# Optimization experiments

Measured on AMD Instinct MI355X. Metric: run time of the kernel, lower is better.

## Reference

```python
import jax, jax.numpy as jnp
import numpy as np

STATE_DIM, ACTION_DIM, HIDDEN_DIM = 12, 4, 16  # hidden_dim must equal state_dim+action_dim
LN_EPS = 1e-5


def setup_inputs() -> dict:
    key = jax.random.key(0)
    ks = jax.random.split(key, 12)
    B, T = 8192, 256
    D = STATE_DIM + ACTION_DIM  # 16
    H = HIDDEN_DIM
    s = 1.0 / np.sqrt(D)
    sh = 1.0 / np.sqrt(H)
    return {
        "initial_state": jax.random.normal(ks[0], (B, 1, STATE_DIM), jnp.float32),
        "commands": jax.random.normal(ks[1], (B, T, ACTION_DIM), jnp.float32),
        "ln_gamma": jnp.ones((D,), jnp.float32),
        "ln_beta": jnp.zeros((D,), jnp.float32),
        "W_in": jax.random.uniform(ks[2], (H, D), jnp.float32, -s, s),
        "b_in": jax.random.uniform(ks[3], (H,), jnp.float32, -s, s),
        "W_ih": jax.random.uniform(ks[4], (4 * H, D), jnp.float32, -sh, sh),  # LSTM input_size = D
        "W_hh": jax.random.uniform(ks[5], (4 * H, H), jnp.float32, -sh, sh),
        "b_ih": jax.random.uniform(ks[6], (4 * H,), jnp.float32, -sh, sh),
        "b_hh": jax.random.uniform(ks[7], (4 * H,), jnp.float32, -sh, sh),
        "W_out": jax.random.uniform(ks[8], (STATE_DIM, H), jnp.float32, -sh, sh),
        "b_out": jax.random.uniform(ks[9], (STATE_DIM,), jnp.float32, -sh, sh),
    }


def _normalize_sincos(state, cos_idx, sin_idx):
    sn, cs = state[:, sin_idx], state[:, cos_idx]
    norm = jnp.sqrt(sn * sn + cs * cs) + 1e-8
    return state.at[:, sin_idx].set(sn / norm).at[:, cos_idx].set(cs / norm)


def _forward(initial_state, commands, ln_gamma, ln_beta, W_in, b_in,
             W_ih, W_hh, b_ih, b_hh, W_out, b_out):
    B = initial_state.shape[0]
    H = W_hh.shape[1]
    state0 = initial_state[:, 0, :]  # (B, S)
    h0 = jnp.zeros((B, H), initial_state.dtype)
    c0 = jnp.zeros((B, H), initial_state.dtype)

    def step(carry, cmd_t):
        state, h, c = carry
        x = jnp.concatenate([state, cmd_t], axis=-1)          # (B, D)
        mu = jnp.mean(x, axis=-1, keepdims=True)
        var = jnp.mean((x - mu) ** 2, axis=-1, keepdims=True)
        x = (x - mu) * jax.lax.rsqrt(var + LN_EPS) * ln_gamma + ln_beta
        x = x @ W_in.T + b_in                                  # (B, H)
        gates = x @ W_ih.T + b_ih + h @ W_hh.T + b_hh          # (B, 4H)
        i, f, g, o = jnp.split(gates, 4, axis=-1)
        c = jax.nn.sigmoid(f) * c + jax.nn.sigmoid(i) * jnp.tanh(g)
        h = jax.nn.sigmoid(o) * jnp.tanh(c)
        state = state + h @ W_out.T + b_out                    # (B, S)
        state = _normalize_sincos(state, 1, 2)
        state = _normalize_sincos(state, 3, 4)
        state = _normalize_sincos(state, 5, 6)
        return (state, h, c), state

    _, outs = jax.lax.scan(step, (state0, h0, c0), jnp.swapaxes(commands, 0, 1))
    return jnp.swapaxes(outs, 0, 1)  # (B, T, S)


def reference(initial_state, commands, ln_gamma, ln_beta, W_in, b_in,
              W_ih, W_hh, b_ih, b_hh, W_out, b_out):
    return _forward(initial_state, commands, ln_gamma, ln_beta, W_in, b_in,
                    W_ih, W_hh, b_ih, b_hh, W_out, b_out)
```

## Files before the change

kernel.cpp:

```cpp
#include <hip/hip_runtime.h>

typedef float f32x2 __attribute__((ext_vector_type(2)));
typedef float f32x4 __attribute__((ext_vector_type(4)));

#define LOG2E 1.44269504088896340736f

__device__ __forceinline__ float rcp_fast(float x) { return __builtin_amdgcn_rcpf(x); }

__device__ __forceinline__ f32x2 mk2(float a, float b) { f32x2 v; v[0] = a; v[1] = b; return v; }

__device__ __forceinline__ float sigmoid_fast(float x) {
    return rcp_fast(1.0f + __builtin_amdgcn_exp2f(-LOG2E * x));
}

__device__ __forceinline__ float tanh_fast(float x) {
    float a = __builtin_fabsf(x);
    float t = __builtin_amdgcn_exp2f(-2.0f * LOG2E * a);
    float r = (1.0f - t) * rcp_fast(1.0f + t);
    return __builtin_copysignf(r, x);
}

__device__ __forceinline__ void load_pairs16(const float* p, f32x2* dst) {
    const f32x4* q4 = (const f32x4*)p;
    f32x4 a = q4[0], b = q4[1], c = q4[2], d = q4[3];
    dst[0] = __builtin_shufflevector(a, a, 0, 1);
    dst[1] = __builtin_shufflevector(a, a, 2, 3);
    dst[2] = __builtin_shufflevector(b, b, 0, 1);
    dst[3] = __builtin_shufflevector(b, b, 2, 3);
    dst[4] = __builtin_shufflevector(c, c, 0, 1);
    dst[5] = __builtin_shufflevector(c, c, 2, 3);
    dst[6] = __builtin_shufflevector(d, d, 0, 1);
    dst[7] = __builtin_shufflevector(d, d, 2, 3);
}

__global__ __launch_bounds__(64, 2) void vm_kernel(
    const float* __restrict__ init_state,
    const float* __restrict__ commands,
    const float* __restrict__ ln_g,
    const float* __restrict__ ln_b,
    const float* __restrict__ W_in,
    const float* __restrict__ b_in,
    const float* __restrict__ W_ih,
    const float* __restrict__ W_hh,
    const float* __restrict__ b_ih,
    const float* __restrict__ b_hh,
    const float* __restrict__ W_out,
    const float* __restrict__ b_out,
    float* __restrict__ out,
    int B, int T)
{
    const int lane = threadIdx.x;
    const int j = lane & 15;
    const int g = lane >> 4;
    const int b = blockIdx.x * 4 + g;

    __shared__ __align__(16) float sh_x[4][24];
    __shared__ __align__(16) float sh_h[4][24];

    f32x2 Wih[4][8], Wh[4][8];
#pragma unroll
    for (int q = 0; q < 4; ++q) {
        load_pairs16(W_ih + (q * 16 + j) * 16, Wih[q]);
        load_pairs16(W_hh + (q * 16 + j) * 16, Wh[q]);
    }

    f32x2 Wgx[4][8];
    float binacc[4];
#pragma unroll
    for (int q = 0; q < 4; ++q) {
        binacc[q] = 0.0f;
#pragma unroll
        for (int k2 = 0; k2 < 8; ++k2) Wgx[q][k2] = mk2(0.0f, 0.0f);
    }
#pragma unroll
    for (int m = 0; m < 16; ++m) {
        f32x2 wm[8];
        load_pairs16(W_in + m * 16, wm);
        float bm = b_in[m];
#pragma unroll
        for (int q = 0; q < 4; ++q) {
            float wim = Wih[q][m >> 1][m & 1];
            f32x2 w2 = mk2(wim, wim);
#pragma unroll
            for (int k2 = 0; k2 < 8; ++k2) Wgx[q][k2] += w2 * wm[k2];
            binacc[q] += wim * bm;
        }
    }
    float sg[4], cst[4];
    {
        f32x2 gg2[8], bt2[8];
        load_pairs16(ln_g, gg2);
        load_pairs16(ln_b, bt2);
#pragma unroll
        for (int q = 0; q < 4; ++q) {
            f32x2 ss = mk2(0.0f, 0.0f), cc = mk2(0.0f, 0.0f);
#pragma unroll
            for (int k2 = 0; k2 < 8; ++k2) {
                cc += Wgx[q][k2] * bt2[k2];
                Wgx[q][k2] *= gg2[k2];
                ss += Wgx[q][k2];
            }
            sg[q]  = ss[0] + ss[1];
            cst[q] = cc[0] + cc[1] + binacc[q] + b_ih[q * 16 + j] + b_hh[q * 16 + j];
        }
    }

    const bool is_state = (j < 12);
    f32x2 Wo[8];
    float bo = 0.0f;
#pragma unroll
    for (int k2 = 0; k2 < 8; ++k2) Wo[k2] = mk2(0.0f, 0.0f);
    if (is_state) {
        load_pairs16(W_out + j * 16, Wo);
        bo = b_out[j];
    }

    float st = is_state ? init_state[b * 12 + j] : 0.0f;
    float c = 0.0f;
    f32x2 hp[8];
#pragma unroll
    for (int k2 = 0; k2 < 8; ++k2) hp[k2] = mk2(0.0f, 0.0f);

    const float* cmd_ptr = commands + (size_t)b * T * 4 + (j >= 12 ? j - 12 : 0);
    float* out_ptr = out + (size_t)b * T * 12 + j;

    int pj = j;
    if (j >= 1 && j <= 6) pj = ((j - 1) ^ 1) + 1;
    const float* ppart = &sh_x[g][pj];
    const bool donorm = (j >= 1 && j <= 6);

    float cmd0 = (j >= 12) ? cmd_ptr[0] : 0.0f;
    sh_x[g][j] = is_state ? st : cmd0;
    f32x2 xp[8];
    load_pairs16(&sh_x[g][0], xp);

    float mu, inv;
    {
        f32x2 s2 = ((xp[0] + xp[1]) + (xp[2] + xp[3])) + ((xp[4] + xp[5]) + (xp[6] + xp[7]));
        float sum = s2[0] + s2[1];
        f32x2 qq = xp[0] * xp[0];
#pragma unroll
        for (int k2 = 1; k2 < 8; ++k2) qq += xp[k2] * xp[k2];
        float sumsq = qq[0] + qq[1];
        mu = sum * 0.0625f;
        float var = sumsq * 0.0625f - mu * mu;
        inv = __builtin_amdgcn_rsqf(var + 1e-5f);
    }

    float cmdS = (j >= 12) ? cmd_ptr[4] : 0.0f;
    float cmdN = (j >= 12) ? cmd_ptr[8] : 0.0f;

    for (int t = 0; t < T; ++t) {
        f32x2 ai = Wgx[0][0] * xp[0], af = Wgx[1][0] * xp[0];
        f32x2 ag = Wgx[2][0] * xp[0], ao = Wgx[3][0] * xp[0];
        f32x2 hi = Wh[0][0] * hp[0], hf = Wh[1][0] * hp[0];
        f32x2 hg = Wh[2][0] * hp[0], ho = Wh[3][0] * hp[0];
#pragma unroll
        for (int k2 = 1; k2 < 8; ++k2) {
            ai += Wgx[0][k2] * xp[k2]; af += Wgx[1][k2] * xp[k2];
            ag += Wgx[2][k2] * xp[k2]; ao += Wgx[3][k2] * xp[k2];
            hi += Wh[0][k2] * hp[k2];  hf += Wh[1][k2] * hp[k2];
            hg += Wh[2][k2] * hp[k2];  ho += Wh[3][k2] * hp[k2];
        }
        float nmi = -mu * inv;
        float gi = __builtin_fmaf(ai[0] + ai[1], inv, __builtin_fmaf(nmi, sg[0], cst[0] + (hi[0] + hi[1])));
        float gf = __builtin_fmaf(af[0] + af[1], inv, __builtin_fmaf(nmi, sg[1], cst[1] + (hf[0] + hf[1])));
        float gG = __builtin_fmaf(ag[0] + ag[1], inv, __builtin_fmaf(nmi, sg[2], cst[2] + (hg[0] + hg[1])));
        float go = __builtin_fmaf(ao[0] + ao[1], inv, __builtin_fmaf(nmi, sg[3], cst[3] + (ho[0] + ho[1])));

        float iv = sigmoid_fast(gi);
        float fv = sigmoid_fast(gf);
        float gv = tanh_fast(gG);
        float ov = sigmoid_fast(go);
        c = fv * c + iv * gv;
        float hv = ov * tanh_fast(c);

        sh_h[g][j] = hv;
        load_pairs16(&sh_h[g][0], hp);

        f32x2 o2 = Wo[0] * hp[0];
#pragma unroll
        for (int k2 = 1; k2 < 8; ++k2) o2 += Wo[k2] * hp[k2];
        float st_raw = st + (o2[0] + o2[1]) + bo;

        sh_x[g][j] = is_state ? st_raw : cmdS;
        float pv = *ppart;
        load_pairs16(&sh_x[g][0], xp);

        float nrm = __builtin_amdgcn_sqrtf(st_raw * st_raw + pv * pv) + 1e-8f;
        float stn = st_raw * rcp_fast(nrm);
        st = donorm ? stn : st_raw;
        if (is_state) out_ptr[0] = st;
        out_ptr += 12;

        {
            float a = xp[0][1], bq = xp[1][0];
            float r = rcp_fast(__builtin_amdgcn_sqrtf(a * a + bq * bq) + 1e-8f);
            xp[0][1] = a * r; xp[1][0] = bq * r;
        }
        {
            float a = xp[1][1], bq = xp[2][0];
            float r = rcp_fast(__builtin_amdgcn_sqrtf(a * a + bq * bq) + 1e-8f);
            xp[1][1] = a * r; xp[2][0] = bq * r;
        }
        {
            float a = xp[2][1], bq = xp[3][0];
            float r = rcp_fast(__builtin_amdgcn_sqrtf(a * a + bq * bq) + 1e-8f);
            xp[2][1] = a * r; xp[3][0] = bq * r;
        }

        f32x2 s2 = ((xp[0] + xp[1]) + (xp[2] + xp[3])) + ((xp[4] + xp[5]) + (xp[6] + xp[7]));
        float sum = s2[0] + s2[1];
        f32x2 qq = xp[0] * xp[0];
#pragma unroll
        for (int k2 = 1; k2 < 8; ++k2) qq += xp[k2] * xp[k2];
        float sumsq = qq[0] + qq[1];
        mu = sum * 0.0625f;
        float var = sumsq * 0.0625f - mu * mu;
        inv = __builtin_amdgcn_rsqf(var + 1e-5f);

        cmdS = cmdN;
        int tn = t + 3;
        if (tn > T - 1) tn = T - 1;
        if (j >= 12) cmdN = cmd_ptr[(size_t)tn * 4];
    }
}

extern "C" void kernel_launch(void* const* d_in, const int* in_sizes, int n_in,
                              void* d_out, int out_size, void* d_ws, size_t ws_size,
                              hipStream_t stream) {
    const float* init_state = (const float*)d_in[0];
    const float* commands   = (const float*)d_in[1];
    const float* ln_g       = (const float*)d_in[2];
    const float* ln_b       = (const float*)d_in[3];
    const float* W_in       = (const float*)d_in[4];
    const float* b_in       = (const float*)d_in[5];
    const float* W_ih       = (const float*)d_in[6];
    const float* W_hh       = (const float*)d_in[7];
    const float* b_ih       = (const float*)d_in[8];
    const float* b_hh       = (const float*)d_in[9];
    const float* W_out      = (const float*)d_in[10];
    const float* b_out      = (const float*)d_in[11];

    int B = in_sizes[0] / 12;
    int T = in_sizes[1] / (B * 4);

    int blocks = B / 4;
    vm_kernel<<<blocks, 64, 0, stream>>>(init_state, commands, ln_g, ln_b,
                                         W_in, b_in, W_ih, W_hh, b_ih, b_hh,
                                         W_out, b_out, (float*)d_out, B, T);
}
```

Before: 364.1 us.

## Compute LSTM gate and output projections with fp16 MFMA over 16 batch rows per wave

```diff
diff --git a/kernel.cpp b/kernel.cpp
--- a/kernel.cpp
+++ b/kernel.cpp
@@ -2,25 +2,42 @@
 
 typedef float f32x2 __attribute__((ext_vector_type(2)));
 typedef float f32x4 __attribute__((ext_vector_type(4)));
+typedef _Float16 f16x4 __attribute__((ext_vector_type(4)));
+typedef __fp16 fp16x2_raw __attribute__((ext_vector_type(2)));
+typedef __fp16 fp16x4_raw __attribute__((ext_vector_type(4)));
 
 #define LOG2E 1.44269504088896340736f
 
-__device__ __forceinline__ float rcp_fast(float x) { return __builtin_amdgcn_rcpf(x); }
-
-__device__ __forceinline__ f32x2 mk2(float a, float b) { f32x2 v; v[0] = a; v[1] = b; return v; }
-
-__device__ __forceinline__ float sigmoid_fast(float x) {
+static __device__ __forceinline__ float rcp_fast(float x) { return __builtin_amdgcn_rcpf(x); }
+
+static __device__ __forceinline__ f32x2 mk2(float a, float b) { f32x2 v; v[0] = a; v[1] = b; return v; }
+
+static __device__ __forceinline__ float sigmoid_fast(float x) {
     return rcp_fast(1.0f + __builtin_amdgcn_exp2f(-LOG2E * x));
 }
 
-__device__ __forceinline__ float tanh_fast(float x) {
+static __device__ __forceinline__ float tanh_fast(float x) {
     float a = __builtin_fabsf(x);
     float t = __builtin_amdgcn_exp2f(-2.0f * LOG2E * a);
     float r = (1.0f - t) * rcp_fast(1.0f + t);
     return __builtin_copysignf(r, x);
 }
 
-__device__ __forceinline__ void load_pairs16(const float* p, f32x2* dst) {
+static __device__ __forceinline__ f16x4 pk4(float a, float b, float c, float d) {
+    fp16x2_raw lo = __builtin_amdgcn_cvt_pkrtz(a, b);
+    fp16x2_raw hi = __builtin_amdgcn_cvt_pkrtz(c, d);
+    fp16x4_raw r = __builtin_shufflevector(lo, hi, 0, 1, 2, 3);
+    return __builtin_bit_cast(f16x4, r);
+}
+
+static __device__ __forceinline__ float swz16(float v) {
+    return __int_as_float(__builtin_amdgcn_ds_swizzle(__float_as_int(v), 0x401F));
+}
+static __device__ __forceinline__ float bperm(int addr, float v) {
+    return __int_as_float(__builtin_amdgcn_ds_bpermute(addr, __float_as_int(v)));
+}
+
+static __device__ __forceinline__ void load_pairs16(const float* p, f32x2* dst) {
     const f32x4* q4 = (const f32x4*)p;
     f32x4 a = q4[0], b = q4[1], c = q4[2], d = q4[3];
     dst[0] = __builtin_shufflevector(a, a, 0, 1);
@@ -33,7 +50,11 @@
     dst[7] = __builtin_shufflevector(d, d, 2, 3);
 }
 
-__global__ __launch_bounds__(64, 2) void vm_kernel(
+#define MFMA16(A, B, C) __builtin_amdgcn_mfma_f32_16x16x16f16(A, B, C, 0, 0, 0)
+#define KSEL(W, half) ((g & 2) ? ((g & 1) ? (W)[6 + (half)] : (W)[4 + (half)]) \
+                               : ((g & 1) ? (W)[2 + (half)] : (W)[0 + (half)]))
+
+__global__ __launch_bounds__(64) void vm_kernel(
     const float* __restrict__ init_state,
     const float* __restrict__ commands,
     const float* __restrict__ ln_g,
@@ -52,18 +73,15 @@
     const int lane = threadIdx.x;
     const int j = lane & 15;
     const int g = lane >> 4;
-    const int b = blockIdx.x * 4 + g;
-
-    __shared__ __align__(16) float sh_x[4][24];
-    __shared__ __align__(16) float sh_h[4][24];
-
-    f32x2 Wih[4][8], Wh[4][8];
+    const int bg = blockIdx.x * 16 + j;
+    const int pa32 = (lane ^ 32) << 2;
+
+    f32x2 Wih[4][8], Wh32[4][8];
 #pragma unroll
     for (int q = 0; q < 4; ++q) {
         load_pairs16(W_ih + (q * 16 + j) * 16, Wih[q]);
-        load_pairs16(W_hh + (q * 16 + j) * 16, Wh[q]);
-    }
-
+        load_pairs16(W_hh + (q * 16 + j) * 16, Wh32[q]);
+    }
     f32x2 Wgx[4][8];
     float binacc[4];
 #pragma unroll
@@ -86,144 +104,153 @@
             binacc[q] += wim * bm;
         }
     }
-    float sg[4], cst[4];
+    float cst[4];
     {
         f32x2 gg2[8], bt2[8];
         load_pairs16(ln_g, gg2);
         load_pairs16(ln_b, bt2);
 #pragma unroll
         for (int q = 0; q < 4; ++q) {
-            f32x2 ss = mk2(0.0f, 0.0f), cc = mk2(0.0f, 0.0f);
+            f32x2 cc2 = mk2(0.0f, 0.0f);
 #pragma unroll
             for (int k2 = 0; k2 < 8; ++k2) {
-                cc += Wgx[q][k2] * bt2[k2];
+                cc2 += Wgx[q][k2] * bt2[k2];
                 Wgx[q][k2] *= gg2[k2];
-                ss += Wgx[q][k2];
             }
-            sg[q]  = ss[0] + ss[1];
-            cst[q] = cc[0] + cc[1] + binacc[q] + b_ih[q * 16 + j] + b_hh[q * 16 + j];
-        }
-    }
-
-    const bool is_state = (j < 12);
-    f32x2 Wo[8];
-    float bo = 0.0f;
-#pragma unroll
-    for (int k2 = 0; k2 < 8; ++k2) Wo[k2] = mk2(0.0f, 0.0f);
-    if (is_state) {
-        load_pairs16(W_out + j * 16, Wo);
-        bo = b_out[j];
-    }
-
-    float st = is_state ? init_state[b * 12 + j] : 0.0f;
-    float c = 0.0f;
-    f32x2 hp[8];
-#pragma unroll
-    for (int k2 = 0; k2 < 8; ++k2) hp[k2] = mk2(0.0f, 0.0f);
-
-    const float* cmd_ptr = commands + (size_t)b * T * 4 + (j >= 12 ? j - 12 : 0);
-    float* out_ptr = out + (size_t)b * T * 12 + j;
-
-    int pj = j;
-    if (j >= 1 && j <= 6) pj = ((j - 1) ^ 1) + 1;
-    const float* ppart = &sh_x[g][pj];
-    const bool donorm = (j >= 1 && j <= 6);
-
-    float cmd0 = (j >= 12) ? cmd_ptr[0] : 0.0f;
-    sh_x[g][j] = is_state ? st : cmd0;
-    f32x2 xp[8];
-    load_pairs16(&sh_x[g][0], xp);
-
-    float mu, inv;
+            cst[q] = cc2[0] + cc2[1] + binacc[q] + b_ih[q * 16 + j] + b_hh[q * 16 + j];
+        }
+    }
+
+    f16x4 Ax[4], Ah[4];
+#pragma unroll
+    for (int q = 0; q < 4; ++q) {
+        f32x2 p0 = KSEL(Wgx[q], 0), p1 = KSEL(Wgx[q], 1);
+        Ax[q] = pk4(p0[0], p0[1], p1[0], p1[1]);
+        f32x2 h0 = KSEL(Wh32[q], 0), h1 = KSEL(Wh32[q], 1);
+        Ah[q] = pk4(h0[0], h0[1], h1[0], h1[1]);
+    }
+    f16x4 Awo;
     {
-        f32x2 s2 = ((xp[0] + xp[1]) + (xp[2] + xp[3])) + ((xp[4] + xp[5]) + (xp[6] + xp[7]));
-        float sum = s2[0] + s2[1];
-        f32x2 qq = xp[0] * xp[0];
-#pragma unroll
-        for (int k2 = 1; k2 < 8; ++k2) qq += xp[k2] * xp[k2];
-        float sumsq = qq[0] + qq[1];
-        mu = sum * 0.0625f;
-        float var = sumsq * 0.0625f - mu * mu;
-        inv = __builtin_amdgcn_rsqf(var + 1e-5f);
-    }
-
-    float cmdS = (j >= 12) ? cmd_ptr[4] : 0.0f;
-    float cmdN = (j >= 12) ? cmd_ptr[8] : 0.0f;
+        f32x2 wo[8];
+#pragma unroll
+        for (int k2 = 0; k2 < 8; ++k2) wo[k2] = mk2(0.0f, 0.0f);
+        if (j < 12) load_pairs16(W_out + j * 16, wo);
+        f32x2 p0 = KSEL(wo, 0), p1 = KSEL(wo, 1);
+        Awo = pk4(p0[0], p0[1], p1[0], p1[1]);
+    }
+
+    __shared__ float cstL[4][16];
+    if (lane < 16) {
+        cstL[0][j] = cst[0]; cstL[1][j] = cst[1];
+        cstL[2][j] = cst[2]; cstL[3][j] = cst[3];
+    }
+    __syncthreads();
+    f32x4 biasv[4];
+#pragma unroll
+    for (int q = 0; q < 4; ++q)
+#pragma unroll
+        for (int r = 0; r < 4; ++r) biasv[q][r] = cstL[q][g * 4 + r];
+
+    const int gg = (g < 3) ? g : 0;
+    f32x4 boV = *(const f32x4*)(b_out + gg * 4);
+    f32x4 stv = *(const f32x4*)(init_state + (size_t)bg * 12 + gg * 4);
+
+    const f32x4* cmd4 = (const f32x4*)(commands + (size_t)bg * T * 4);
+    float* outp = out + (size_t)bg * T * 12 + g * 4;
+    const bool isg3 = (g == 3);
+
+    f32x4 cmdS = {0.f, 0.f, 0.f, 0.f}, cmdN = {0.f, 0.f, 0.f, 0.f};
+    if (isg3) {
+        f32x4 c0 = cmd4[0];
+        stv = c0;
+        cmdS = cmd4[(T > 1) ? 1 : 0];
+        cmdN = cmd4[(T > 2) ? 2 : 0];
+    }
+
+#define LN_XFRAG(xf)                                                          \
+    do {                                                                      \
+        float _ps = (stv[0] + stv[1]) + (stv[2] + stv[3]);                    \
+        float _pq = ((stv[0] * stv[0] + stv[1] * stv[1]) +                    \
+                     (stv[2] * stv[2] + stv[3] * stv[3]));                    \
+        _ps += swz16(_ps); _pq += swz16(_pq);                                 \
+        _ps += bperm(pa32, _ps); _pq += bperm(pa32, _pq);                     \
+        float _mu = _ps * 0.0625f;                                            \
+        float _var = _pq * 0.0625f - _mu * _mu;                               \
+        float _inv = __builtin_amdgcn_rsqf(_var + 1e-5f);                     \
+        float _nmi = -_mu * _inv;                                             \
+        xf = pk4(__builtin_fmaf(stv[0], _inv, _nmi),                          \
+                 __builtin_fmaf(stv[1], _inv, _nmi),                          \
+                 __builtin_fmaf(stv[2], _inv, _nmi),                          \
+                 __builtin_fmaf(stv[3], _inv, _nmi));                         \
+    } while (0)
+
+    f16x4 xfrag, hfrag = pk4(0.f, 0.f, 0.f, 0.f);
+    LN_XFRAG(xfrag);
+
+    f32x4 cc = {0.f, 0.f, 0.f, 0.f};
 
     for (int t = 0; t < T; ++t) {
-        f32x2 ai = Wgx[0][0] * xp[0], af = Wgx[1][0] * xp[0];
-        f32x2 ag = Wgx[2][0] * xp[0], ao = Wgx[3][0] * xp[0];
-        f32x2 hi = Wh[0][0] * hp[0], hf = Wh[1][0] * hp[0];
-        f32x2 hg = Wh[2][0] * hp[0], ho = Wh[3][0] * hp[0];
-#pragma unroll
-        for (int k2 = 1; k2 < 8; ++k2) {
-            ai += Wgx[0][k2] * xp[k2]; af += Wgx[1][k2] * xp[k2];
-            ag += Wgx[2][k2] * xp[k2]; ao += Wgx[3][k2] * xp[k2];
-            hi += Wh[0][k2] * hp[k2];  hf += Wh[1][k2] * hp[k2];
-            hg += Wh[2][k2] * hp[k2];  ho += Wh[3][k2] * hp[k2];
-        }
-        float nmi = -mu * inv;
-        float gi = __builtin_fmaf(ai[0] + ai[1], inv, __builtin_fmaf(nmi, sg[0], cst[0] + (hi[0] + hi[1])));
-        float gf = __builtin_fmaf(af[0] + af[1], inv, __builtin_fmaf(nmi, sg[1], cst[1] + (hf[0] + hf[1])));
-        float gG = __builtin_fmaf(ag[0] + ag[1], inv, __builtin_fmaf(nmi, sg[2], cst[2] + (hg[0] + hg[1])));
-        float go = __builtin_fmaf(ao[0] + ao[1], inv, __builtin_fmaf(nmi, sg[3], cst[3] + (ho[0] + ho[1])));
-
-        float iv = sigmoid_fast(gi);
-        float fv = sigmoid_fast(gf);
-        float gv = tanh_fast(gG);
-        float ov = sigmoid_fast(go);
-        c = fv * c + iv * gv;
-        float hv = ov * tanh_fast(c);
-
-        sh_h[g][j] = hv;
-        load_pairs16(&sh_h[g][0], hp);
-
-        f32x2 o2 = Wo[0] * hp[0];
-#pragma unroll
-        for (int k2 = 1; k2 < 8; ++k2) o2 += Wo[k2] * hp[k2];
-        float st_raw = st + (o2[0] + o2[1]) + bo;
-
-        sh_x[g][j] = is_state ? st_raw : cmdS;
-        float pv = *ppart;
-        load_pairs16(&sh_x[g][0], xp);
-
-        float nrm = __builtin_amdgcn_sqrtf(st_raw * st_raw + pv * pv) + 1e-8f;
-        float stn = st_raw * rcp_fast(nrm);
-        st = donorm ? stn : st_raw;
-        if (is_state) out_ptr[0] = st;
-        out_ptr += 12;
-
+        f32x4 a0 = MFMA16(Ax[0], xfrag, biasv[0]);
+        f32x4 a1 = MFMA16(Ax[1], xfrag, biasv[1]);
+        f32x4 a2 = MFMA16(Ax[2], xfrag, biasv[2]);
+        f32x4 a3 = MFMA16(Ax[3], xfrag, biasv[3]);
+        a0 = MFMA16(Ah[0], hfrag, a0);
+        a1 = MFMA16(Ah[1], hfrag, a1);
+        a2 = MFMA16(Ah[2], hfrag, a2);
+        a3 = MFMA16(Ah[3], hfrag, a3);
+
+        float hv0, hv1, hv2, hv3;
         {
-            float a = xp[0][1], bq = xp[1][0];
-            float r = rcp_fast(__builtin_amdgcn_sqrtf(a * a + bq * bq) + 1e-8f);
-            xp[0][1] = a * r; xp[1][0] = bq * r;
-        }
-        {
-            float a = xp[1][1], bq = xp[2][0];
-            float r = rcp_fast(__builtin_amdgcn_sqrtf(a * a + bq * bq) + 1e-8f);
-            xp[1][1] = a * r; xp[2][0] = bq * r;
-        }
-        {
-            float a = xp[2][1], bq = xp[3][0];
-            float r = rcp_fast(__builtin_amdgcn_sqrtf(a * a + bq * bq) + 1e-8f);
-            xp[2][1] = a * r; xp[3][0] = bq * r;
-        }
-
-        f32x2 s2 = ((xp[0] + xp[1]) + (xp[2] + xp[3])) + ((xp[4] + xp[5]) + (xp[6] + xp[7]));
-        float sum = s2[0] + s2[1];
-        f32x2 qq = xp[0] * xp[0];
-#pragma unroll
-        for (int k2 = 1; k2 < 8; ++k2) qq += xp[k2] * xp[k2];
-        float sumsq = qq[0] + qq[1];
-        mu = sum * 0.0625f;
-        float var = sumsq * 0.0625f - mu * mu;
-        inv = __builtin_amdgcn_rsqf(var + 1e-5f);
+            float iv, fv, gv, ov;
+            iv = sigmoid_fast(a0[0]); fv = sigmoid_fast(a1[0]);
+            gv = tanh_fast(a2[0]);    ov = sigmoid_fast(a3[0]);
+            cc[0] = fv * cc[0] + iv * gv; hv0 = ov * tanh_fast(cc[0]);
+            iv = sigmoid_fast(a0[1]); fv = sigmoid_fast(a1[1]);
+            gv = tanh_fast(a2[1]);    ov = sigmoid_fast(a3[1]);
+            cc[1] = fv * cc[1] + iv * gv; hv1 = ov * tanh_fast(cc[1]);
+            iv = sigmoid_fast(a0[2]); fv = sigmoid_fast(a1[2]);
+            gv = tanh_fast(a2[2]);    ov = sigmoid_fast(a3[2]);
+            cc[2] = fv * cc[2] + iv * gv; hv2 = ov * tanh_fast(cc[2]);
+            iv = sigmoid_fast(a0[3]); fv = sigmoid_fast(a1[3]);
+            gv = tanh_fast(a2[3]);    ov = sigmoid_fast(a3[3]);
+            cc[3] = fv * cc[3] + iv * gv; hv3 = ov * tanh_fast(cc[3]);
+        }
+        hfrag = pk4(hv0, hv1, hv2, hv3);
+
+        f32x4 cw;
+        cw[0] = stv[0] + boV[0]; cw[1] = stv[1] + boV[1];
+        cw[2] = stv[2] + boV[2]; cw[3] = stv[3] + boV[3];
+        f32x4 so = MFMA16(Awo, hfrag, cw);
+
+        float s0 = so[0], s1 = so[1], s2 = so[2], s3 = so[3];
+        float ex = (g == 1) ? s0 : s3;
+        float px = swz16(ex);
+        bool g01 = (g <= 1);
+        float r12 = rcp_fast(__builtin_amdgcn_sqrtf(s1 * s1 + s2 * s2) + 1e-8f);
+        s1 = g01 ? s1 * r12 : s1;
+        s2 = g01 ? s2 * r12 : s2;
+        float aa = (g == 1) ? s0 : s3;
+        float rcr = rcp_fast(__builtin_amdgcn_sqrtf(aa * aa + px * px) + 1e-8f);
+        s3 = (g == 0) ? s3 * rcr : s3;
+        s0 = (g == 1) ? s0 * rcr : s0;
+
+        if (g < 3) {
+            f32x4 ov4; ov4[0] = s0; ov4[1] = s1; ov4[2] = s2; ov4[3] = s3;
+            *(f32x4*)outp = ov4;
+        }
+        outp += 12;
+
+        f32x4 nx; nx[0] = s0; nx[1] = s1; nx[2] = s2; nx[3] = s3;
+        if (isg3) nx = cmdS;
+        stv = nx;
+        LN_XFRAG(xfrag);
 
         cmdS = cmdN;
         int tn = t + 3;
         if (tn > T - 1) tn = T - 1;
-        if (j >= 12) cmdN = cmd_ptr[(size_t)tn * 4];
-    }
+        if (isg3) cmdN = cmd4[tn];
+    }
+#undef LN_XFRAG
 }
 
 extern "C" void kernel_launch(void* const* d_in, const int* in_sizes, int n_in,
@@ -245,7 +272,7 @@
     int B = in_sizes[0] / 12;
     int T = in_sizes[1] / (B * 4);
 
-    int blocks = B / 4;
+    int blocks = B / 16;
     vm_kernel<<<blocks, 64, 0, stream>>>(init_state, commands, ln_g, ln_b,
                                          W_in, b_in, W_ih, W_hh, b_ih, b_hh,
                                          W_out, b_out, (float*)d_out, B, T);
```

Result: faster. 320.5 us (-12.0%).
